# Kernel tuning notes

Hardware: AMD Instinct MI355X
Metric: run time of the kernel (lower is better)

The kernel has to match this reference:

```python
import jax, jax.numpy as jnp
import numpy as np

H = 256  # GRU hidden size


def _gru_scan(state, lengths, Wih, Whh, bih, bhh):
    # state: [B, T, D]; run a batched GRU over time, freezing h once t >= lengths[b]
    B, T, D = state.shape
    # precompute input gates for all timesteps: [T, B, 3H]
    gi_all = jnp.einsum('btd,gd->tbg', state, Wih) + bih

    def step(h, inp):
        gi, t = inp
        gh = h @ Whh.T + bhh                       # [B, 3H]
        i_r, i_z, i_n = jnp.split(gi, 3, axis=-1)
        h_r, h_z, h_n = jnp.split(gh, 3, axis=-1)
        r = jax.nn.sigmoid(i_r + h_r)
        z = jax.nn.sigmoid(i_z + h_z)
        n = jnp.tanh(i_n + r * h_n)
        h_new = (1.0 - z) * n + z * h              # torch GRUCell update
        mask = (t < lengths)[:, None]              # ragged: stop updating past length
        return jnp.where(mask, h_new, h), None

    h0 = jnp.zeros((B, H), state.dtype)
    h, _ = jax.lax.scan(step, h0, (gi_all, jnp.arange(T)))
    return h  # [B, H] = hidden after lengths[b] GRU steps


def _mlp(x, w1, b1, w2, b2, w3, b3, w4, b4, wq, bq):
    x = jax.nn.relu(x @ w1.T + b1)
    x = jax.nn.relu(x @ w2.T + b2)
    x = jax.nn.relu(x @ w3.T + b3)
    x = jax.nn.relu(x @ w4.T + b4)
    return x @ wq.T + bq  # [B, 1]


def setup_inputs() -> dict:
    key = jax.random.key(0)
    ks = jax.random.split(key, 40)
    B, T, D, A = 2048, 64, 15, 1
    inp = {}
    inp['state'] = jax.random.normal(ks[0], (B, T, D), jnp.float32)
    inp['action'] = jax.random.normal(ks[1], (B, A), jnp.float32)
    inp['lengths'] = jax.random.randint(ks[2], (B,), 1, T + 1, jnp.int32)
    i = 3
    for t in (1, 2):
        for name, shape, fan in [('Wih', (3 * H, D), D), ('Whh', (3 * H, H), H),
                                 ('bih', (3 * H,), H), ('bhh', (3 * H,), H)]:
            inp[f'g{t}_{name}'] = jax.random.normal(ks[i], shape, jnp.float32) / np.sqrt(fan)
            i += 1
        for name, (o, n) in [('fc1', (1024, H + D + A)), ('fc2', (1024, 1024)),
                             ('fc3', (512, 1024)), ('fc4', (256, 512)), ('q', (1, 256))]:
            inp[f'{name}_{t}_w'] = jax.random.normal(ks[i], (o, n), jnp.float32) / np.sqrt(n)
            i += 1
            inp[f'{name}_{t}_b'] = jax.random.normal(ks[i], (o,), jnp.float32) * 0.01
            i += 1
    return inp


def reference(state, action, lengths,
              g1_Wih, g1_Whh, g1_bih, g1_bhh,
              fc1_1_w, fc1_1_b, fc2_1_w, fc2_1_b, fc3_1_w, fc3_1_b,
              fc4_1_w, fc4_1_b, q_1_w, q_1_b,
              g2_Wih, g2_Whh, g2_bih, g2_bhh,
              fc1_2_w, fc1_2_b, fc2_2_w, fc2_2_b, fc3_2_w, fc3_2_b,
              fc4_2_w, fc4_2_b, q_2_w, q_2_b):
    h1 = _gru_scan(state, lengths, g1_Wih, g1_Whh, g1_bih, g1_bhh)
    h2 = _gru_scan(state, lengths, g2_Wih, g2_Whh, g2_bih, g2_bhh)
    aug = jnp.concatenate([state[:, 0, :], action], axis=-1)  # [B, 16]
    x1 = jnp.concatenate([aug, h1], axis=-1)                  # [B, 272]
    x2 = jnp.concatenate([aug, h2], axis=-1)
    out1 = _mlp(x1, fc1_1_w, fc1_1_b, fc2_1_w, fc2_1_b, fc3_1_w, fc3_1_b,
                fc4_1_w, fc4_1_b, q_1_w, q_1_b)
    out2 = _mlp(x2, fc1_2_w, fc1_2_b, fc2_2_w, fc2_2_b, fc3_2_w, fc3_2_b,
                fc4_2_w, fc4_2_b, q_2_w, q_2_b)
    return (out1, out2)
```

## Files before the change

### kernel.cpp

```cpp
#include <hip/hip_runtime.h>

typedef float  f32x4 __attribute__((ext_vector_type(4)));
typedef short  s16x8 __attribute__((ext_vector_type(8)));
typedef __bf16 b16x8 __attribute__((ext_vector_type(8)));

#define DEV __device__ __forceinline__

DEV unsigned short f2b(float f) {
  unsigned u = __builtin_bit_cast(unsigned, f);
  u = (u + 0x7FFFu + ((u >> 16) & 1u)) >> 16;
  return (unsigned short)u;
}
DEV b16x8 ld8(const unsigned short* p) {
  return __builtin_bit_cast(b16x8, *(const s16x8*)p);
}
DEV float sigm(float x) { return __builtin_amdgcn_rcpf(1.f + __expf(-x)); }
DEV float tanh_fast(float x) {
  float e = __expf(2.f * x);
  return 1.f - 2.f * __builtin_amdgcn_rcpf(e + 1.f);
}
DEV void async16(const unsigned short* g, unsigned short* l) {
  __builtin_amdgcn_global_load_lds(
      (const __attribute__((address_space(1))) unsigned int*)g,
      (__attribute__((address_space(3))) unsigned int*)l, 16, 0, 0);
}
DEV f32x4 mfma_bf16(b16x8 a, b16x8 b, f32x4 c) {
  return __builtin_amdgcn_mfma_f32_16x16x32_bf16(a, b, c, 0, 0, 0);
}

struct PrepArgs {
  const float *whh[2], *wih[2], *bih[2], *bhh[2];
  const float *src[2][4];
  unsigned short *waug[2], *dst[2][4];
  const float *qb[2];
  float *out;
};

__global__ __launch_bounds__(256) void prep_kernel(PrepArgs p) {
  const int job = blockIdx.y;
  const int i0 = blockIdx.x * 256 + threadIdx.x;
  const int stride = gridDim.x * 256;
  if (job < 2) {
    const float* whh = p.whh[job];
    const float* wih = p.wih[job];
    const float* bih = p.bih[job];
    const float* bhh = p.bhh[job];
    unsigned short* dst = p.waug[job];
    for (int idx = i0; idx < 768 * 288; idx += stride) {
      int j = idx / 288, k = idx - j * 288;
      float v = 0.f;
      if (k < 256) {
        int o = k & 31;
        int kk = (k & 0x1E0) + (o >> 1) + ((o & 1) << 4);
        v = whh[j * 256 + kk];
      } else if (k < 271)  v = wih[j * 15 + (k - 256)];
      else if (k == 271)   v = (j < 512) ? (bih[j] + bhh[j]) : bih[j];
      dst[idx] = f2b(v);
    }
  } else if (job < 10) {
    const int jj = job - 2, br = jj >> 2, ly = jj & 3;
    const int rowsA[4] = {1024, 1024, 512, 256};
    const int scA[4]   = {272, 1024, 1024, 512};
    const int dcA[4]   = {288, 1024, 1024, 512};
    const float* src = p.src[br][ly];
    unsigned short* dst = p.dst[br][ly];
    const int sc = scA[ly], dc = dcA[ly], tot = rowsA[ly] * dc;
    for (int idx = i0; idx < tot; idx += stride) {
      int r = idx / dc, c = idx - r * dc;
      float v = (c < sc) ? src[r * sc + c] : 0.f;
      dst[idx] = f2b(v);
    }
  } else {
    for (int idx = i0; idx < 4096; idx += stride)
      p.out[idx] = p.qb[idx >> 11][0];
  }
}

#define GRU_LDS_BYTES 147584
__global__ __launch_bounds__(512) void gru_kernel(
    const float* __restrict__ state, const float* __restrict__ action,
    const int* __restrict__ lengths,
    const unsigned short* __restrict__ waug0, const unsigned short* __restrict__ waug1,
    const float* __restrict__ bhh0, const float* __restrict__ bhh1,
    unsigned short* __restrict__ x0, unsigned short* __restrict__ x1) {
  extern __shared__ char smem[];
  unsigned short* W67L = (unsigned short*)smem;
  unsigned short* SgL  = (unsigned short*)(smem + 98304);
  unsigned*       Hb2  = (unsigned*)(smem + 131072);
  int* lenS = (int*)(smem + 147456);
  int* mlS  = (int*)(smem + 147520);
  float* tmpF = (float*)smem;

  const int tid = threadIdx.x;
  const int lane = tid & 63, w = tid >> 6;
  const int l15 = lane & 15, q = lane >> 4;
  const int g = blockIdx.x & 1;
  const int r0 = (blockIdx.x >> 1) * 16;

  const unsigned short* Waug = g ? waug1 : waug0;
  const float* bhh = g ? bhh1 : bhh0;
  unsigned short* xout = g ? x1 : x0;

  {
    const float4* src = (const float4*)(state + (size_t)r0 * 960);
    float4* dstv = (float4*)tmpF;
    for (int i = tid; i < 3840; i += 512) dstv[i] = src[i];
  }
  for (int i = tid; i < 4096; i += 512) Hb2[i] = 0;
  if (tid < 16) lenS[tid] = lengths[r0 + tid];
  __syncthreads();
  if (tid == 0) {
    int m = 1;
    for (int i = 0; i < 16; i++) m = lenS[i] > m ? lenS[i] : m;
    *mlS = m;
  }

  for (int s = tid; s < 64 * 32; s += 512) {
    const int t = s >> 5, L = s & 31;
    const int q2 = L >> 4, r = L & 15;
    s16x8 h;
#pragma unroll
    for (int j = 0; j < 8; j++) {
      const int k = q2 * 8 + j;
      float v = (k < 15) ? tmpF[r * 960 + t * 15 + k] : (k == 15 ? 1.0f : 0.f);
      h[j] = (short)f2b(v);
    }
    *(s16x8*)(SgL + (size_t)s * 8) = h;
  }
  __syncthreads();

  int c0[6];
  c0[0] = 32 * w;       c0[1] = 32 * w + 16;
  c0[2] = 256 + 32 * w; c0[3] = 256 + 32 * w + 16;
  c0[4] = 512 + 32 * w; c0[5] = 512 + 32 * w + 16;

  b16x8 wres[6][6];
  b16x8 waugf[6];
#pragma unroll
  for (int i = 0; i < 6; i++) {
    const unsigned short* bpi = Waug + (size_t)(c0[i] + l15) * 288 + q * 8;
#pragma unroll
    for (int j = 0; j < 6; j++) wres[i][j] = ld8(bpi + j * 32);
    waugf[i] = ld8(bpi + 256);
#pragma unroll
    for (int ks2 = 0; ks2 < 2; ks2++) {
      b16x8 v = ld8(bpi + (6 + ks2) * 32);
      *(s16x8*)(W67L + (size_t)(ks2 * 6 + i) * 4096 + tid * 8) =
          __builtin_bit_cast(s16x8, v);
    }
  }
  float bnH[2] = {bhh[c0[4] + l15], bhh[c0[5] + l15]};
  int len4[4];
#pragma unroll
  for (int r = 0; r < 4; r++) len4[r] = lenS[q * 4 + r];

  int aOff[8];
#pragma unroll
  for (int j = 0; j < 8; j++) {
    const int cj = 4 * j + q;
    const int pj = (cj & 24) | ((cj & 7) ^ (l15 & 7));
    aOff[j] = l15 * 128 + pj * 4;
  }
  int wOff[4];
#pragma unroll
  for (int rg = 0; rg < 4; rg++) {
    const int row = q * 4 + rg;
    const int cb = 4 * w + (l15 >> 2);
    const int pw = (cb & 24) | ((cb & 7) ^ (row & 7));
    wOff[rg] = row * 128 + pw * 4 + (l15 & 3);
  }
  __syncthreads();
  const int maxlen = *mlS;

  float hold[2][4] = {{0, 0, 0, 0}, {0, 0, 0, 0}};
  const short qmask = (q < 2) ? (short)-1 : (short)0;
  const s16x8 qm = {qmask, qmask, qmask, qmask, qmask, qmask, qmask, qmask};
  int poff = 0;

  for (int t = 0; t < maxlen; ++t) {
    __syncthreads();

    f32x4 acc[6];
#pragma unroll
    for (int i = 0; i < 6; i++) acc[i] = f32x4{0.f, 0.f, 0.f, 0.f};

    {
      s16x8 raw = *(const s16x8*)(SgL + t * 256 + ((q & 1) * 16 + l15) * 8);
      raw &= qm;
      b16x8 a8 = __builtin_bit_cast(b16x8, raw);
#pragma unroll
      for (int i = 0; i < 6; i++) acc[i] = mfma_bf16(a8, waugf[i], acc[i]);
    }
    f32x4 giN0 = acc[4], giN1 = acc[5];
    acc[4] = acc[4] + bnH[0];
    acc[5] = acc[5] + bnH[1];

    const unsigned* hb = Hb2 + poff;
#pragma unroll
    for (int j = 0; j < 6; j++) {
      b16x8 a = __builtin_bit_cast(b16x8, *(const uint4*)(hb + aOff[j]));
#pragma unroll
      for (int i = 0; i < 6; i++) acc[i] = mfma_bf16(a, wres[i][j], acc[i]);
    }
#pragma unroll
    for (int ks2 = 0; ks2 < 2; ks2++) {
      b16x8 a = __builtin_bit_cast(b16x8, *(const uint4*)(hb + aOff[6 + ks2]));
#pragma unroll
      for (int i = 0; i < 6; i++) {
        b16x8 bw = ld8(W67L + (size_t)(ks2 * 6 + i) * 4096 + tid * 8);
        acc[i] = mfma_bf16(a, bw, acc[i]);
      }
    }

    unsigned* hbw = Hb2 + (poff ^ 2048);
#pragma unroll
    for (int rg = 0; rg < 4; rg++) {
      const bool live = (t < len4[rg]);
      float r0g = sigm(acc[0][rg]);
      float z0 = sigm(acc[2][rg]);
      float n0 = tanh_fast(giN0[rg] + r0g * (acc[4][rg] - giN0[rg]));
      float h0 = n0 + z0 * (hold[0][rg] - n0);
      h0 = live ? h0 : hold[0][rg];
      hold[0][rg] = h0;
      float r1g = sigm(acc[1][rg]);
      float z1 = sigm(acc[3][rg]);
      float n1 = tanh_fast(giN1[rg] + r1g * (acc[5][rg] - giN1[rg]));
      float h1 = n1 + z1 * (hold[1][rg] - n1);
      h1 = live ? h1 : hold[1][rg];
      hold[1][rg] = h1;
      hbw[wOff[rg]] = (unsigned)f2b(h0) | ((unsigned)f2b(h1) << 16);
    }
    poff ^= 2048;
  }

#pragma unroll
  for (int i = 0; i < 2; i++) {
    const int c = 32 * w + 16 * i + l15;
#pragma unroll
    for (int rg = 0; rg < 4; rg++) {
      const int row = q * 4 + rg;
      xout[(size_t)(r0 + row) * 288 + 16 + c] = f2b(hold[i][rg]);
    }
  }
  {
    const int row = tid >> 5, cc = tid & 31;
    float v; int col;
    if (cc < 15)       { v = state[(size_t)(r0 + row) * 960 + cc]; col = cc; }
    else if (cc == 15) { v = action[r0 + row]; col = 15; }
    else               { v = 0.f; col = 256 + cc; }
    xout[(size_t)(r0 + row) * 288 + col] = f2b(v);
  }
}

template <int BM, int BN>
__global__ __launch_bounds__(256, 2) void gemm_bias_relu(
    const unsigned short* __restrict__ A0, const unsigned short* __restrict__ A1,
    const unsigned short* __restrict__ W0, const unsigned short* __restrict__ W1,
    const float* __restrict__ b0, const float* __restrict__ b1,
    unsigned short* __restrict__ Y0, unsigned short* __restrict__ Y1,
    int N, int K) {
  const unsigned short* A = blockIdx.z ? A1 : A0;
  const unsigned short* W = blockIdx.z ? W1 : W0;
  const float* bias = blockIdx.z ? b1 : b0;
  unsigned short* Y = blockIdx.z ? Y1 : Y0;

  constexpr int MT = BM / 32;
  constexpr int NT = BN / 32;
  const int tid = threadIdx.x;
  const int lane = tid & 63, wid = tid >> 6;
  const int wm = wid >> 1, wn = wid & 1;
  const int l15 = lane & 15, q = lane >> 4;
  const int m0 = blockIdx.x * BM, n0 = blockIdx.y * BN;

  __shared__ unsigned short As[BM * 32];
  __shared__ unsigned short Bs[BN * 32];

  f32x4 acc[MT][NT];
#pragma unroll
  for (int mi = 0; mi < MT; mi++)
#pragma unroll
    for (int ni = 0; ni < NT; ni++) acc[mi][ni] = f32x4{0.f, 0.f, 0.f, 0.f};

  const int srow = tid >> 2, scol = (tid & 3) * 8;

  for (int k0 = 0; k0 < K; k0 += 32) {
#pragma unroll
    for (int g64 = 0; g64 < BM / 64; g64++)
      async16(A + (size_t)(m0 + g64 * 64 + srow) * K + scol + k0,
              &As[g64 * 2048 + tid * 8]);
#pragma unroll
    for (int g64 = 0; g64 < BN / 64; g64++)
      async16(W + (size_t)(n0 + g64 * 64 + srow) * K + scol + k0,
              &Bs[g64 * 2048 + tid * 8]);
    __syncthreads();

    b16x8 af[MT], bf[NT];
#pragma unroll
    for (int mi = 0; mi < MT; mi++)
      af[mi] = ld8(&As[(wm * (BM / 2) + mi * 16 + l15) * 32 + q * 8]);
#pragma unroll
    for (int ni = 0; ni < NT; ni++)
      bf[ni] = ld8(&Bs[(wn * (BN / 2) + ni * 16 + l15) * 32 + q * 8]);
#pragma unroll
    for (int mi = 0; mi < MT; mi++)
#pragma unroll
      for (int ni = 0; ni < NT; ni++)
        acc[mi][ni] = mfma_bf16(af[mi], bf[ni], acc[mi][ni]);
    __syncthreads();
  }

#pragma unroll
  for (int ni = 0; ni < NT; ni++) {
    const int col = n0 + wn * (BN / 2) + ni * 16 + l15;
    const float bv = bias[col];
#pragma unroll
    for (int mi = 0; mi < MT; mi++) {
      const int rbase = m0 + wm * (BM / 2) + mi * 16 + q * 4;
#pragma unroll
      for (int rg = 0; rg < 4; rg++) {
        float v = acc[mi][ni][rg] + bv;
        v = fmaxf(v, 0.f);
        Y[(size_t)(rbase + rg) * N + col] = f2b(v);
      }
    }
  }
}

__global__ __launch_bounds__(256, 2) void fc4q_kernel(
    const unsigned short* __restrict__ A0, const unsigned short* __restrict__ A1,
    const unsigned short* __restrict__ W0, const unsigned short* __restrict__ W1,
    const float* __restrict__ b0, const float* __restrict__ b1,
    const float* __restrict__ qw0, const float* __restrict__ qw1,
    float* __restrict__ out) {
  const unsigned short* A = blockIdx.z ? A1 : A0;
  const unsigned short* W = blockIdx.z ? W1 : W0;
  const float* bias = blockIdx.z ? b1 : b0;
  const float* qw = blockIdx.z ? qw1 : qw0;

  const int tid = threadIdx.x;
  const int lane = tid & 63, wn = tid >> 6;
  const int l15 = lane & 15, q = lane >> 4;
  const int m0 = blockIdx.x * 32;
  const int nbase = blockIdx.y * 128;
  const int K = 512;

  __shared__ unsigned short As[32 * 32];
  __shared__ unsigned short Bs[128 * 32];
  __shared__ float red[32][4];

  f32x4 acc[2][2];
#pragma unroll
  for (int mi = 0; mi < 2; mi++)
#pragma unroll
    for (int ni = 0; ni < 2; ni++) acc[mi][ni] = f32x4{0.f, 0.f, 0.f, 0.f};

  const int srow = tid >> 2, scol = (tid & 3) * 8;
  for (int k0 = 0; k0 < K; k0 += 32) {
    if (tid < 128)
      async16(A + (size_t)(m0 + srow) * K + scol + k0, &As[tid * 8]);
#pragma unroll
    for (int g64 = 0; g64 < 2; g64++)
      async16(W + (size_t)(nbase + g64 * 64 + srow) * K + scol + k0,
              &Bs[g64 * 2048 + tid * 8]);
    __syncthreads();

    b16x8 af[2], bf[2];
#pragma unroll
    for (int mi = 0; mi < 2; mi++)
      af[mi] = ld8(&As[(mi * 16 + l15) * 32 + q * 8]);
#pragma unroll
    for (int ni = 0; ni < 2; ni++)
      bf[ni] = ld8(&Bs[(wn * 32 + ni * 16 + l15) * 32 + q * 8]);
#pragma unroll
    for (int mi = 0; mi < 2; mi++)
#pragma unroll
      for (int ni = 0; ni < 2; ni++)
        acc[mi][ni] = mfma_bf16(af[mi], bf[ni], acc[mi][ni]);
    __syncthreads();
  }

#pragma unroll
  for (int mi = 0; mi < 2; mi++) {
#pragma unroll
    for (int rg = 0; rg < 4; rg++) {
      float s = 0.f;
#pragma unroll
      for (int ni = 0; ni < 2; ni++) {
        const int col = nbase + wn * 32 + ni * 16 + l15;
        float v = fmaxf(acc[mi][ni][rg] + bias[col], 0.f);
        s += v * qw[col];
      }
#pragma unroll
      for (int off = 1; off < 16; off <<= 1) s += __shfl_xor(s, off);
      if (l15 == 0) red[mi * 16 + q * 4 + rg][wn] = s;
    }
  }
  __syncthreads();
  if (tid < 32) {
    float t = red[tid][0] + red[tid][1] + red[tid][2] + red[tid][3];
    atomicAdd(out + (size_t)blockIdx.z * 2048 + m0 + tid, t);
  }
}

extern "C" void kernel_launch(void* const* d_in, const int* in_sizes, int n_in,
                              void* d_out, int out_size, void* d_ws, size_t ws_size,
                              hipStream_t stream) {
  const float* state   = (const float*)d_in[0];
  const float* action  = (const float*)d_in[1];
  const int*   lengths = (const int*)d_in[2];
  const float* g_wih[2] = {(const float*)d_in[3], (const float*)d_in[17]};
  const float* g_whh[2] = {(const float*)d_in[4], (const float*)d_in[18]};
  const float* g_bih[2] = {(const float*)d_in[5], (const float*)d_in[19]};
  const float* g_bhh[2] = {(const float*)d_in[6], (const float*)d_in[20]};
  const float* fcw[2][4] = {
      {(const float*)d_in[7], (const float*)d_in[9], (const float*)d_in[11], (const float*)d_in[13]},
      {(const float*)d_in[21], (const float*)d_in[23], (const float*)d_in[25], (const float*)d_in[27]}};
  const float* fcb[2][4] = {
      {(const float*)d_in[8], (const float*)d_in[10], (const float*)d_in[12], (const float*)d_in[14]},
      {(const float*)d_in[22], (const float*)d_in[24], (const float*)d_in[26], (const float*)d_in[28]}};
  const float* qw[2] = {(const float*)d_in[15], (const float*)d_in[29]};
  const float* qb[2] = {(const float*)d_in[16], (const float*)d_in[30]};
  float* out = (float*)d_out;

  uintptr_t base = (uintptr_t)d_ws;
  auto alloc = [&](size_t bytes) -> unsigned short* {
    void* p = (void*)base;
    base += (bytes + 255) & ~(size_t)255;
    return (unsigned short*)p;
  };
  unsigned short *waug[2], *w1b[2], *w2b[2], *w3b[2], *w4b[2], *xb[2], *yA[2], *yB[2];
  for (int g = 0; g < 2; g++) waug[g] = alloc(768 * 288 * 2);
  for (int g = 0; g < 2; g++) w1b[g] = alloc(1024 * 288 * 2);
  for (int g = 0; g < 2; g++) w2b[g] = alloc(1024 * 1024 * 2);
  for (int g = 0; g < 2; g++) w3b[g] = alloc(512 * 1024 * 2);
  for (int g = 0; g < 2; g++) w4b[g] = alloc(256 * 512 * 2);
  for (int g = 0; g < 2; g++) xb[g] = alloc(2048 * 288 * 2);
  for (int g = 0; g < 2; g++) yA[g] = alloc(2048 * 1024 * 2);
  for (int g = 0; g < 2; g++) yB[g] = alloc(2048 * 1024 * 2);
  (void)ws_size; (void)in_sizes; (void)n_in; (void)out_size;

  PrepArgs pa;
  for (int g = 0; g < 2; g++) {
    pa.whh[g] = g_whh[g]; pa.wih[g] = g_wih[g];
    pa.bih[g] = g_bih[g]; pa.bhh[g] = g_bhh[g];
    pa.waug[g] = waug[g];
    pa.src[g][0] = fcw[g][0]; pa.dst[g][0] = w1b[g];
    pa.src[g][1] = fcw[g][1]; pa.dst[g][1] = w2b[g];
    pa.src[g][2] = fcw[g][2]; pa.dst[g][2] = w3b[g];
    pa.src[g][3] = fcw[g][3]; pa.dst[g][3] = w4b[g];
    pa.qb[g] = qb[g];
  }
  pa.out = out;
  prep_kernel<<<dim3(64, 11), 256, 0, stream>>>(pa);

  (void)hipFuncSetAttribute((const void*)gru_kernel,
                            hipFuncAttributeMaxDynamicSharedMemorySize,
                            GRU_LDS_BYTES);
  gru_kernel<<<dim3(256), dim3(512), GRU_LDS_BYTES, stream>>>(
      state, action, lengths, waug[0], waug[1], g_bhh[0], g_bhh[1], xb[0], xb[1]);

  gemm_bias_relu<128, 128><<<dim3(16, 8, 2), 256, 0, stream>>>(
      xb[0], xb[1], w1b[0], w1b[1], fcb[0][0], fcb[1][0], yA[0], yA[1], 1024, 288);
  gemm_bias_relu<128, 128><<<dim3(16, 8, 2), 256, 0, stream>>>(
      yA[0], yA[1], w2b[0], w2b[1], fcb[0][1], fcb[1][1], yB[0], yB[1], 1024, 1024);
  gemm_bias_relu<128, 64><<<dim3(16, 8, 2), 256, 0, stream>>>(
      yB[0], yB[1], w3b[0], w3b[1], fcb[0][2], fcb[1][2], yA[0], yA[1], 512, 1024);
  fc4q_kernel<<<dim3(64, 2, 2), 256, 0, stream>>>(
      yA[0], yA[1], w4b[0], w4b[1], fcb[0][3], fcb[1][3], qw[0], qw[1], out);
}
```

Before: 332.1 us.

## Double-buffer MLP GEMM tiles and trim GRU step overhead with packed bf16 converts

The fc GEMM and fc4q kernels now double-buffer their LDS tiles, so the async global-to-LDS load of the next K slice is issued while MFMAs run on the current one. In the GRU kernel, the per-step barrier moves after the input-gate MFMAs so they can overlap the wait. The qmask AND is dropped and the accumulator zeroing is folded into the first MFMA. Hardware v_cvt_pk_bf16_f32 replaces the manual bf16 rounding, and the staged state rows are padded to avoid LDS bank conflicts. The GRU launch bound now asks for 2 blocks per CU, which may force register spills given its large register-resident weights; double buffering also doubles GEMM LDS use.

```diff
diff --git a/kernel.cpp b/kernel.cpp
--- a/kernel.cpp
+++ b/kernel.cpp
@@ -3,6 +3,7 @@
 typedef float  f32x4 __attribute__((ext_vector_type(4)));
 typedef short  s16x8 __attribute__((ext_vector_type(8)));
 typedef __bf16 b16x8 __attribute__((ext_vector_type(8)));
+typedef unsigned u32x4 __attribute__((ext_vector_type(4)));
 
 #define DEV __device__ __forceinline__
 
@@ -10,6 +11,11 @@
   unsigned u = __builtin_bit_cast(unsigned, f);
   u = (u + 0x7FFFu + ((u >> 16) & 1u)) >> 16;
   return (unsigned short)u;
+}
+DEV unsigned cvt_pk_bf16(float lo, float hi) {
+  unsigned r;
+  asm("v_cvt_pk_bf16_f32 %0, %1, %2" : "=v"(r) : "v"(lo), "v"(hi));
+  return r;
 }
 DEV b16x8 ld8(const unsigned short* p) {
   return __builtin_bit_cast(b16x8, *(const s16x8*)p);
@@ -77,7 +83,7 @@
 }
 
 #define GRU_LDS_BYTES 147584
-__global__ __launch_bounds__(512) void gru_kernel(
+__global__ __launch_bounds__(512, 2) void gru_kernel(
     const float* __restrict__ state, const float* __restrict__ action,
     const int* __restrict__ lengths,
     const unsigned short* __restrict__ waug0, const unsigned short* __restrict__ waug1,
@@ -104,7 +110,10 @@
   {
     const float4* src = (const float4*)(state + (size_t)r0 * 960);
     float4* dstv = (float4*)tmpF;
-    for (int i = tid; i < 3840; i += 512) dstv[i] = src[i];
+    for (int i = tid; i < 3840; i += 512) {
+      const int row = i / 240;
+      dstv[row * 241 + (i - row * 240)] = src[i];
+    }
   }
   for (int i = tid; i < 4096; i += 512) Hb2[i] = 0;
   if (tid < 16) lenS[tid] = lengths[r0 + tid];
@@ -118,14 +127,16 @@
   for (int s = tid; s < 64 * 32; s += 512) {
     const int t = s >> 5, L = s & 31;
     const int q2 = L >> 4, r = L & 15;
-    s16x8 h;
-#pragma unroll
-    for (int j = 0; j < 8; j++) {
-      const int k = q2 * 8 + j;
-      float v = (k < 15) ? tmpF[r * 960 + t * 15 + k] : (k == 15 ? 1.0f : 0.f);
-      h[j] = (short)f2b(v);
-    }
-    *(s16x8*)(SgL + (size_t)s * 8) = h;
+    const float* bp = tmpF + r * 964 + t * 15;
+    unsigned hp[4];
+#pragma unroll
+    for (int jp = 0; jp < 4; jp++) {
+      const int k0 = q2 * 8 + 2 * jp;
+      float lo = (k0 < 15) ? bp[k0] : (k0 == 15 ? 1.0f : 0.f);
+      float hi = (k0 + 1 < 15) ? bp[k0 + 1] : (k0 + 1 == 15 ? 1.0f : 0.f);
+      hp[jp] = cvt_pk_bf16(lo, hi);
+    }
+    *(u32x4*)(SgL + (size_t)s * 8) = u32x4{hp[0], hp[1], hp[2], hp[3]};
   }
   __syncthreads();
 
@@ -173,27 +184,22 @@
   const int maxlen = *mlS;
 
   float hold[2][4] = {{0, 0, 0, 0}, {0, 0, 0, 0}};
-  const short qmask = (q < 2) ? (short)-1 : (short)0;
-  const s16x8 qm = {qmask, qmask, qmask, qmask, qmask, qmask, qmask, qmask};
   int poff = 0;
 
   for (int t = 0; t < maxlen; ++t) {
-    __syncthreads();
-
     f32x4 acc[6];
-#pragma unroll
-    for (int i = 0; i < 6; i++) acc[i] = f32x4{0.f, 0.f, 0.f, 0.f};
-
     {
       s16x8 raw = *(const s16x8*)(SgL + t * 256 + ((q & 1) * 16 + l15) * 8);
-      raw &= qm;
       b16x8 a8 = __builtin_bit_cast(b16x8, raw);
-#pragma unroll
-      for (int i = 0; i < 6; i++) acc[i] = mfma_bf16(a8, waugf[i], acc[i]);
+      const f32x4 z4 = {0.f, 0.f, 0.f, 0.f};
+#pragma unroll
+      for (int i = 0; i < 6; i++) acc[i] = mfma_bf16(a8, waugf[i], z4);
     }
     f32x4 giN0 = acc[4], giN1 = acc[5];
     acc[4] = acc[4] + bnH[0];
     acc[5] = acc[5] + bnH[1];
+
+    __syncthreads();
 
     const unsigned* hb = Hb2 + poff;
 #pragma unroll
@@ -228,7 +234,7 @@
       float h1 = n1 + z1 * (hold[1][rg] - n1);
       h1 = live ? h1 : hold[1][rg];
       hold[1][rg] = h1;
-      hbw[wOff[rg]] = (unsigned)f2b(h0) | ((unsigned)f2b(h1) << 16);
+      hbw[wOff[rg]] = cvt_pk_bf16(h0, h1);
     }
     poff ^= 2048;
   }
@@ -272,8 +278,8 @@
   const int l15 = lane & 15, q = lane >> 4;
   const int m0 = blockIdx.x * BM, n0 = blockIdx.y * BN;
 
-  __shared__ unsigned short As[BM * 32];
-  __shared__ unsigned short Bs[BN * 32];
+  __shared__ unsigned short As[2][BM * 32];
+  __shared__ unsigned short Bs[2][BN * 32];
 
   f32x4 acc[MT][NT];
 #pragma unroll
@@ -282,25 +288,39 @@
     for (int ni = 0; ni < NT; ni++) acc[mi][ni] = f32x4{0.f, 0.f, 0.f, 0.f};
 
   const int srow = tid >> 2, scol = (tid & 3) * 8;
-
-  for (int k0 = 0; k0 < K; k0 += 32) {
-#pragma unroll
-    for (int g64 = 0; g64 < BM / 64; g64++)
-      async16(A + (size_t)(m0 + g64 * 64 + srow) * K + scol + k0,
-              &As[g64 * 2048 + tid * 8]);
-#pragma unroll
-    for (int g64 = 0; g64 < BN / 64; g64++)
-      async16(W + (size_t)(n0 + g64 * 64 + srow) * K + scol + k0,
-              &Bs[g64 * 2048 + tid * 8]);
-    __syncthreads();
+  const int nk = K >> 5;
+
+#pragma unroll
+  for (int g64 = 0; g64 < BM / 64; g64++)
+    async16(A + (size_t)(m0 + g64 * 64 + srow) * K + scol,
+            &As[0][g64 * 2048 + tid * 8]);
+#pragma unroll
+  for (int g64 = 0; g64 < BN / 64; g64++)
+    async16(W + (size_t)(n0 + g64 * 64 + srow) * K + scol,
+            &Bs[0][g64 * 2048 + tid * 8]);
+  __syncthreads();
+
+  for (int t = 0; t < nk; ++t) {
+    const int cur = t & 1;
+    if (t + 1 < nk) {
+      const int k1 = (t + 1) * 32;
+#pragma unroll
+      for (int g64 = 0; g64 < BM / 64; g64++)
+        async16(A + (size_t)(m0 + g64 * 64 + srow) * K + scol + k1,
+                &As[cur ^ 1][g64 * 2048 + tid * 8]);
+#pragma unroll
+      for (int g64 = 0; g64 < BN / 64; g64++)
+        async16(W + (size_t)(n0 + g64 * 64 + srow) * K + scol + k1,
+                &Bs[cur ^ 1][g64 * 2048 + tid * 8]);
+    }
 
     b16x8 af[MT], bf[NT];
 #pragma unroll
     for (int mi = 0; mi < MT; mi++)
-      af[mi] = ld8(&As[(wm * (BM / 2) + mi * 16 + l15) * 32 + q * 8]);
+      af[mi] = ld8(&As[cur][(wm * (BM / 2) + mi * 16 + l15) * 32 + q * 8]);
 #pragma unroll
     for (int ni = 0; ni < NT; ni++)
-      bf[ni] = ld8(&Bs[(wn * (BN / 2) + ni * 16 + l15) * 32 + q * 8]);
+      bf[ni] = ld8(&Bs[cur][(wn * (BN / 2) + ni * 16 + l15) * 32 + q * 8]);
 #pragma unroll
     for (int mi = 0; mi < MT; mi++)
 #pragma unroll
@@ -344,8 +364,8 @@
   const int nbase = blockIdx.y * 128;
   const int K = 512;
 
-  __shared__ unsigned short As[32 * 32];
-  __shared__ unsigned short Bs[128 * 32];
+  __shared__ unsigned short As[2][32 * 32];
+  __shared__ unsigned short Bs[2][128 * 32];
   __shared__ float red[32][4];
 
   f32x4 acc[2][2];
@@ -355,22 +375,35 @@
     for (int ni = 0; ni < 2; ni++) acc[mi][ni] = f32x4{0.f, 0.f, 0.f, 0.f};
 
   const int srow = tid >> 2, scol = (tid & 3) * 8;
-  for (int k0 = 0; k0 < K; k0 += 32) {
-    if (tid < 128)
-      async16(A + (size_t)(m0 + srow) * K + scol + k0, &As[tid * 8]);
-#pragma unroll
-    for (int g64 = 0; g64 < 2; g64++)
-      async16(W + (size_t)(nbase + g64 * 64 + srow) * K + scol + k0,
-              &Bs[g64 * 2048 + tid * 8]);
-    __syncthreads();
+  const int nk = K >> 5;
+
+  if (tid < 128)
+    async16(A + (size_t)(m0 + srow) * K + scol, &As[0][tid * 8]);
+#pragma unroll
+  for (int g64 = 0; g64 < 2; g64++)
+    async16(W + (size_t)(nbase + g64 * 64 + srow) * K + scol,
+            &Bs[0][g64 * 2048 + tid * 8]);
+  __syncthreads();
+
+  for (int t = 0; t < nk; ++t) {
+    const int cur = t & 1;
+    if (t + 1 < nk) {
+      const int k1 = (t + 1) * 32;
+      if (tid < 128)
+        async16(A + (size_t)(m0 + srow) * K + scol + k1, &As[cur ^ 1][tid * 8]);
+#pragma unroll
+      for (int g64 = 0; g64 < 2; g64++)
+        async16(W + (size_t)(nbase + g64 * 64 + srow) * K + scol + k1,
+                &Bs[cur ^ 1][g64 * 2048 + tid * 8]);
+    }
 
     b16x8 af[2], bf[2];
 #pragma unroll
     for (int mi = 0; mi < 2; mi++)
-      af[mi] = ld8(&As[(mi * 16 + l15) * 32 + q * 8]);
+      af[mi] = ld8(&As[cur][(mi * 16 + l15) * 32 + q * 8]);
 #pragma unroll
     for (int ni = 0; ni < 2; ni++)
-      bf[ni] = ld8(&Bs[(wn * 32 + ni * 16 + l15) * 32 + q * 8]);
+      bf[ni] = ld8(&Bs[cur][(wn * 32 + ni * 16 + l15) * 32 + q * 8]);
 #pragma unroll
     for (int mi = 0; mi < 2; mi++)
 #pragma unroll
```

After: 316.8 us. 4.6% less time.
